# Kernel optimization log

Hardware: AMD Instinct MI355X
Metric: run time of the kernel (lower is better)

The kernel has to match this reference:

```python
import jax, jax.numpy as jnp
import numpy as np

N_NODES = 50000
N_EDGES = 1600000
IN_CH = 128
HID = 128
OUT_CH = 2
N_GRAPHS = 512
N_HID_LAYERS = 5  # first 5 SAGEConv+BN+ReLU blocks; 6th conv has no BN/act
EPS = 1e-5


def setup_inputs() -> dict:
    key = jax.random.key(0)
    ks = jax.random.split(key, 13)
    x = jax.random.normal(ks[0], (N_NODES, IN_CH), jnp.float32)
    edge_index = jax.random.randint(ks[1], (2, N_EDGES), 0, N_NODES)
    batch = jnp.sort(jax.random.randint(ks[2], (N_NODES,), 0, N_GRAPHS))
    s = 1.0 / np.sqrt(HID)
    # SAGEConv params for the 5 hidden layers (in==hid==128 so they stack)
    Wl = jax.random.normal(ks[3], (N_HID_LAYERS, HID, HID), jnp.float32) * s  # lin_l (neighbors)
    Wr = jax.random.normal(ks[4], (N_HID_LAYERS, HID, HID), jnp.float32) * s  # lin_r (root)
    b = jax.random.normal(ks[5], (N_HID_LAYERS, HID), jnp.float32) * s
    # BatchNorm (eval mode: running stats + affine)
    gamma = 1.0 + 0.1 * jax.random.normal(ks[6], (N_HID_LAYERS, HID), jnp.float32)
    beta = 0.1 * jax.random.normal(ks[7], (N_HID_LAYERS, HID), jnp.float32)
    rmean = 0.1 * jax.random.normal(ks[8], (N_HID_LAYERS, HID), jnp.float32)
    rvar = 0.5 + jax.random.uniform(ks[9], (N_HID_LAYERS, HID), dtype=jnp.float32)
    # final SAGEConv: hid -> out
    Wl_out = jax.random.normal(ks[10], (HID, OUT_CH), jnp.float32) * s
    Wr_out = jax.random.normal(ks[11], (HID, OUT_CH), jnp.float32) * s
    b_out = jax.random.normal(ks[12], (OUT_CH,), jnp.float32) * s
    return dict(x=x, Wl=Wl, Wr=Wr, b=b, gamma=gamma, beta=beta, rmean=rmean,
                rvar=rvar, Wl_out=Wl_out, Wr_out=Wr_out, b_out=b_out,
                edge_index=edge_index, batch=batch)


def reference(x, Wl, Wr, b, gamma, beta, rmean, rvar, Wl_out, Wr_out, b_out,
              edge_index, batch):
    src, dst = edge_index[0], edge_index[1]
    # in-degree for mean aggregation (shared across all layers)
    deg = jax.ops.segment_sum(jnp.ones((src.shape[0],), x.dtype), dst,
                              num_segments=N_NODES)
    inv_deg = (1.0 / jnp.maximum(deg, 1.0))[:, None]  # [N,1]

    def sage(h, Wl_, Wr_, b_):
        # PyG SAGEConv: lin_l(mean_{j in N(i)} x_j) + lin_r(x_i)
        agg = jax.ops.segment_sum(h[src], dst, num_segments=N_NODES) * inv_deg
        return agg @ Wl_ + h @ Wr_ + b_

    h = x
    for l in range(N_HID_LAYERS):
        h = sage(h, Wl[l], Wr[l], b[l])
        # BatchNorm1d in eval mode: affine with running stats
        h = (h - rmean[l]) * (gamma[l] * jax.lax.rsqrt(rvar[l] + EPS)) + beta[l]
        h = jax.nn.relu(h)
        # F.dropout(p=0.2, training=False) is identity in eval
    h = sage(h, Wl_out, Wr_out, b_out)  # [N, OUT_CH]
    # global_mean_pool over graphs
    gsum = jax.ops.segment_sum(h, batch, num_segments=N_GRAPHS)
    gcnt = jax.ops.segment_sum(jnp.ones((h.shape[0],), h.dtype), batch,
                               num_segments=N_GRAPHS)
    return gsum / jnp.maximum(gcnt, 1.0)[:, None]  # [N_GRAPHS, OUT_CH]
```

## Files before the change

### kernel.cpp

```cpp
#include <hip/hip_runtime.h>

#define HID 128
#define BN_EPS 1e-5f

typedef short bf16x8 __attribute__((ext_vector_type(8)));
typedef float f32x4 __attribute__((ext_vector_type(4)));

__device__ inline unsigned short f2b(float f) {
  unsigned int u = __float_as_uint(f);
  unsigned int r = (u + 0x7fffu + ((u >> 16) & 1u)) >> 16;
  return (unsigned short)r;
}
__device__ inline float bl(unsigned int v) { return __uint_as_float(v << 16); }
__device__ inline float bh(unsigned int v) { return __uint_as_float(v & 0xffff0000u); }


__global__ void k_bhist(const int* __restrict__ dst, int* __restrict__ bcnt, int e, int nb) {
  __shared__ int h[256];
  for (int i = threadIdx.x; i < 256; i += blockDim.x) h[i] = 0;
  __syncthreads();
  int stride = gridDim.x * blockDim.x;
  for (int i = blockIdx.x * blockDim.x + threadIdx.x; i < e; i += stride)
    atomicAdd(&h[dst[i] >> 8], 1);
  __syncthreads();
  for (int i = threadIdx.x; i < nb; i += blockDim.x)
    if (h[i]) atomicAdd(&bcnt[i], h[i]);
}

__global__ void k_bscan(const int* __restrict__ bcnt, int* __restrict__ base,
                        int* __restrict__ cur, int nb) {
  __shared__ int ws[4];
  int t = threadIdx.x;
  int v = (t < nb) ? bcnt[t] : 0;
  int lane = t & 63, wid = t >> 6;
  int x = v;
#pragma unroll
  for (int off = 1; off < 64; off <<= 1) {
    int y = __shfl_up(x, off, 64);
    if (lane >= off) x += y;
  }
  if (lane == 63) ws[wid] = x;
  __syncthreads();
  int add = 0;
  for (int w = 0; w < wid; ++w) add += ws[w];
  int incl = x + add;
  int excl = incl - v;
  if (t < nb) { base[t] = excl; cur[t] = excl; }
  if (t == nb - 1) base[nb] = incl;
}

__global__ void k_bscatter(const int* __restrict__ src, const int* __restrict__ dst,
                           int* __restrict__ cur, uint2* __restrict__ binned, int e) {
  __shared__ int bc[256];
  __shared__ int bo[256];
  int nchunk = (e + gridDim.x - 1) / gridDim.x;
  int c0 = blockIdx.x * nchunk;
  int c1 = min(c0 + nchunk, e);
  for (int i = threadIdx.x; i < 256; i += blockDim.x) bc[i] = 0;
  __syncthreads();
  for (int i = c0 + threadIdx.x; i < c1; i += blockDim.x)
    atomicAdd(&bc[dst[i] >> 8], 1);
  __syncthreads();
  for (int i = threadIdx.x; i < 256; i += blockDim.x) {
    int c = bc[i];
    bo[i] = c ? atomicAdd(&cur[i], c) : 0;
    bc[i] = 0;
  }
  __syncthreads();
  for (int i = c0 + threadIdx.x; i < c1; i += blockDim.x) {
    int d = dst[i];
    int b = d >> 8;
    int pos = bo[b] + atomicAdd(&bc[b], 1);
    binned[pos] = make_uint2((unsigned)src[i], (unsigned)d);
  }
}

__global__ __launch_bounds__(256) void k_bfill(
    const uint2* __restrict__ binned, const int* __restrict__ base,
    int* __restrict__ row_ptr, float* __restrict__ inv_deg,
    int* __restrict__ col, int n, int nb) {
  __shared__ int cnt[256];
  __shared__ int cur[256];
  __shared__ int ws[4];
  int b = blockIdx.x;
  int t = threadIdx.x;
  int n0 = b << 8;
  int e0 = base[b], e1 = base[b + 1];
  cnt[t] = 0;
  __syncthreads();
  for (int i = e0 + t; i < e1; i += 256)
    atomicAdd(&cnt[binned[i].y & 255], 1);
  __syncthreads();
  int v = cnt[t];
  int lane = t & 63, wid = t >> 6;
  int x = v;
#pragma unroll
  for (int off = 1; off < 64; off <<= 1) {
    int y = __shfl_up(x, off, 64);
    if (lane >= off) x += y;
  }
  if (lane == 63) ws[wid] = x;
  __syncthreads();
  int add = 0;
  for (int w = 0; w < wid; ++w) add += ws[w];
  int excl = x - v + add;
  int node = n0 + t;
  if (node < n) {
    row_ptr[node] = e0 + excl;
    inv_deg[node] = 1.0f / (float)max(v, 1);
  }
  cur[t] = e0 + excl;
  __syncthreads();
  for (int i = e0 + t; i < e1; i += 256) {
    uint2 pr = binned[i];
    int pos = atomicAdd(&cur[pr.y & 255], 1);
    col[pos] = (int)pr.x;
  }
  if (b == 0 && t == 0) row_ptr[n] = base[nb];
}


__global__ void k_prep(const float* __restrict__ x, unsigned short* __restrict__ xb,
                       const float* __restrict__ Wl, const float* __restrict__ Wr,
                       unsigned short* __restrict__ Wlt, unsigned short* __restrict__ Wrt,
                       const float* __restrict__ g, const float* __restrict__ be,
                       const float* __restrict__ rm, const float* __restrict__ rv,
                       float* __restrict__ sc, float* __restrict__ sh,
                       int n4, int wtot, int bn) {
  int i = blockIdx.x * blockDim.x + threadIdx.x;
  if (i < n4) {
    float4 v = ((const float4*)x)[i];
    unsigned int lo = (unsigned int)f2b(v.x) | ((unsigned int)f2b(v.y) << 16);
    unsigned int hi = (unsigned int)f2b(v.z) | ((unsigned int)f2b(v.w) << 16);
    ((uint2*)xb)[i] = make_uint2(lo, hi);
  } else if (i < n4 + wtot) {
    int j = i - n4;
    int mat = j >> 14, rem = j & 16383, nn = rem >> 7, kk = rem & 127;
    int sidx = (mat << 14) + (kk << 7) + nn;
    Wlt[j] = f2b(Wl[sidx]);
    Wrt[j] = f2b(Wr[sidx]);
  } else if (i < n4 + wtot + bn) {
    int j = i - n4 - wtot;
    float s = g[j] * rsqrtf(rv[j] + BN_EPS);
    sc[j] = s;
    sh[j] = be[j] - rm[j] * s;
  }
}


__global__ __launch_bounds__(256) void k_spmm_g(
    const unsigned short* __restrict__ hbsrc, const int* __restrict__ row_ptr,
    const int* __restrict__ col, const float* __restrict__ inv_deg,
    unsigned short* __restrict__ aggb, int n) {
  int node = blockIdx.x * 4 + (threadIdx.x >> 6);
  if (node >= n) return;
  int lane = threadIdx.x & 63;
  int slot = lane >> 4, c16 = lane & 15;
  int beg = row_ptr[node], end = row_ptr[node + 1];
  float a0 = 0, a1 = 0, a2 = 0, a3 = 0, a4 = 0, a5 = 0, a6 = 0, a7 = 0;
  const unsigned short* base = hbsrc + (c16 << 3);
  int e = beg;
  for (; e + 16 <= end; e += 16) {
    int s0 = col[e + slot];
    int s1 = col[e + 4 + slot];
    int s2 = col[e + 8 + slot];
    int s3 = col[e + 12 + slot];
    uint4 v0 = *(const uint4*)(base + ((size_t)s0 << 7));
    uint4 v1 = *(const uint4*)(base + ((size_t)s1 << 7));
    uint4 v2 = *(const uint4*)(base + ((size_t)s2 << 7));
    uint4 v3 = *(const uint4*)(base + ((size_t)s3 << 7));
    a0 += bl(v0.x); a1 += bh(v0.x); a2 += bl(v0.y); a3 += bh(v0.y);
    a4 += bl(v0.z); a5 += bh(v0.z); a6 += bl(v0.w); a7 += bh(v0.w);
    a0 += bl(v1.x); a1 += bh(v1.x); a2 += bl(v1.y); a3 += bh(v1.y);
    a4 += bl(v1.z); a5 += bh(v1.z); a6 += bl(v1.w); a7 += bh(v1.w);
    a0 += bl(v2.x); a1 += bh(v2.x); a2 += bl(v2.y); a3 += bh(v2.y);
    a4 += bl(v2.z); a5 += bh(v2.z); a6 += bl(v2.w); a7 += bh(v2.w);
    a0 += bl(v3.x); a1 += bh(v3.x); a2 += bl(v3.y); a3 += bh(v3.y);
    a4 += bl(v3.z); a5 += bh(v3.z); a6 += bl(v3.w); a7 += bh(v3.w);
  }
  for (; e < end; e += 4) {
    int idx = e + slot;
    if (idx < end) {
      int s = col[idx];
      uint4 v = *(const uint4*)(base + ((size_t)s << 7));
      a0 += bl(v.x); a1 += bh(v.x); a2 += bl(v.y); a3 += bh(v.y);
      a4 += bl(v.z); a5 += bh(v.z); a6 += bl(v.w); a7 += bh(v.w);
    }
  }
#pragma unroll
  for (int st = 16; st <= 32; st <<= 1) {
    a0 += __shfl_xor(a0, st); a1 += __shfl_xor(a1, st);
    a2 += __shfl_xor(a2, st); a3 += __shfl_xor(a3, st);
    a4 += __shfl_xor(a4, st); a5 += __shfl_xor(a5, st);
    a6 += __shfl_xor(a6, st); a7 += __shfl_xor(a7, st);
  }
  if (slot == 0) {
    float w = inv_deg[node];
    unsigned int p0 = (unsigned int)f2b(a0 * w) | ((unsigned int)f2b(a1 * w) << 16);
    unsigned int p1 = (unsigned int)f2b(a2 * w) | ((unsigned int)f2b(a3 * w) << 16);
    unsigned int p2 = (unsigned int)f2b(a4 * w) | ((unsigned int)f2b(a5 * w) << 16);
    unsigned int p3 = (unsigned int)f2b(a6 * w) | ((unsigned int)f2b(a7 * w) << 16);
    *(uint4*)(aggb + ((size_t)node << 7) + (c16 << 3)) = make_uint4(p0, p1, p2, p3);
  }
}


__global__ __launch_bounds__(256) void k_gemm3(
    const unsigned short* __restrict__ aggb,
    const unsigned short* __restrict__ hbsrc,
    const unsigned short* __restrict__ Wlt,
    const unsigned short* __restrict__ Wrt,
    const float* __restrict__ bias, const float* __restrict__ sc,
    const float* __restrict__ sh, unsigned short* __restrict__ hbo,
    int n, int ngroups) {
  int w = threadIdx.x >> 6;
  int lane = threadIdx.x & 63;
  int l15 = lane & 15, lhi = lane >> 4;

  bf16x8 aL[2][4], aR[2][4];
#pragma unroll
  for (int ms = 0; ms < 2; ++ms) {
    int row = (w << 5) + (ms << 4) + l15;
#pragma unroll
    for (int ks = 0; ks < 4; ++ks) {
      aL[ms][ks] = *(const bf16x8*)(Wlt + (row << 7) + (ks << 5) + (lhi << 3));
      aR[ms][ks] = *(const bf16x8*)(Wrt + (row << 7) + (ks << 5) + (lhi << 3));
    }
  }
  float4 bi[2], scv[2], shv[2];
#pragma unroll
  for (int ms = 0; ms < 2; ++ms) {
    int ch = (w << 5) + (ms << 4) + (lhi << 2);
    bi[ms] = *(const float4*)(bias + ch);
    scv[ms] = *(const float4*)(sc + ch);
    shv[ms] = *(const float4*)(sh + ch);
  }

  for (int g = blockIdx.x; g < ngroups; g += gridDim.x) {
    int node = (g << 4) + l15;
    bool ok = node < n;
    int nsafe = ok ? node : 0;
    const unsigned short* arow = aggb + ((size_t)nsafe << 7) + (lhi << 3);
    const unsigned short* hrow = hbsrc + ((size_t)nsafe << 7) + (lhi << 3);
    bf16x8 bA0 = *(const bf16x8*)(arow);
    bf16x8 bA1 = *(const bf16x8*)(arow + 32);
    bf16x8 bA2 = *(const bf16x8*)(arow + 64);
    bf16x8 bA3 = *(const bf16x8*)(arow + 96);
    bf16x8 bH0 = *(const bf16x8*)(hrow);
    bf16x8 bH1 = *(const bf16x8*)(hrow + 32);
    bf16x8 bH2 = *(const bf16x8*)(hrow + 64);
    bf16x8 bH3 = *(const bf16x8*)(hrow + 96);
    f32x4 acc[2];
#pragma unroll
    for (int ms = 0; ms < 2; ++ms) acc[ms] = (f32x4)(0.f);
#pragma unroll
    for (int ms = 0; ms < 2; ++ms) {
      acc[ms] = __builtin_amdgcn_mfma_f32_16x16x32_bf16(aL[ms][0], bA0, acc[ms], 0, 0, 0);
      acc[ms] = __builtin_amdgcn_mfma_f32_16x16x32_bf16(aL[ms][1], bA1, acc[ms], 0, 0, 0);
      acc[ms] = __builtin_amdgcn_mfma_f32_16x16x32_bf16(aL[ms][2], bA2, acc[ms], 0, 0, 0);
      acc[ms] = __builtin_amdgcn_mfma_f32_16x16x32_bf16(aL[ms][3], bA3, acc[ms], 0, 0, 0);
      acc[ms] = __builtin_amdgcn_mfma_f32_16x16x32_bf16(aR[ms][0], bH0, acc[ms], 0, 0, 0);
      acc[ms] = __builtin_amdgcn_mfma_f32_16x16x32_bf16(aR[ms][1], bH1, acc[ms], 0, 0, 0);
      acc[ms] = __builtin_amdgcn_mfma_f32_16x16x32_bf16(aR[ms][2], bH2, acc[ms], 0, 0, 0);
      acc[ms] = __builtin_amdgcn_mfma_f32_16x16x32_bf16(aR[ms][3], bH3, acc[ms], 0, 0, 0);
    }
    if (ok) {
#pragma unroll
      for (int ms = 0; ms < 2; ++ms) {
        int ch = (w << 5) + (ms << 4) + (lhi << 2);
        float o0 = fmaxf((acc[ms][0] + bi[ms].x) * scv[ms].x + shv[ms].x, 0.f);
        float o1 = fmaxf((acc[ms][1] + bi[ms].y) * scv[ms].y + shv[ms].y, 0.f);
        float o2 = fmaxf((acc[ms][2] + bi[ms].z) * scv[ms].z + shv[ms].z, 0.f);
        float o3 = fmaxf((acc[ms][3] + bi[ms].w) * scv[ms].w + shv[ms].w, 0.f);
        unsigned int lo = (unsigned int)f2b(o0) | ((unsigned int)f2b(o1) << 16);
        unsigned int hi = (unsigned int)f2b(o2) | ((unsigned int)f2b(o3) << 16);
        *(uint2*)(hbo + ((size_t)node << 7) + ch) = make_uint2(lo, hi);
      }
    }
  }
}


__global__ void k_pq(const unsigned short* __restrict__ hb, const float* __restrict__ Wl_out,
                     const float* __restrict__ Wr_out, float* __restrict__ p,
                     float* __restrict__ q, int n) {
  int node = blockIdx.x * 4 + (threadIdx.x >> 6);
  if (node >= n) return;
  int lane = threadIdx.x & 63;
  unsigned int hv = *(const unsigned int*)(hb + ((size_t)node << 7) + (lane << 1));
  float hx = bl(hv), hy = bh(hv);
  float4 wl = *(const float4*)(Wl_out + (lane << 2));
  float4 wr = *(const float4*)(Wr_out + (lane << 2));
  float p0 = hx * wl.x + hy * wl.z;
  float p1 = hx * wl.y + hy * wl.w;
  float q0 = hx * wr.x + hy * wr.z;
  float q1 = hx * wr.y + hy * wr.w;
#pragma unroll
  for (int off = 32; off > 0; off >>= 1) {
    p0 += __shfl_xor(p0, off, 64);
    p1 += __shfl_xor(p1, off, 64);
    q0 += __shfl_xor(q0, off, 64);
    q1 += __shfl_xor(q1, off, 64);
  }
  if (lane == 0) {
    *(float2*)(p + (size_t)node * 2) = make_float2(p0, p1);
    *(float2*)(q + (size_t)node * 2) = make_float2(q0, q1);
  }
}

__global__ void k_spmm2p(const float* __restrict__ p, const float* __restrict__ q,
                         const int* __restrict__ row_ptr, const int* __restrict__ col,
                         const float* __restrict__ inv_deg, const float* __restrict__ b_out,
                         const int* __restrict__ batch, float* __restrict__ out,
                         float* __restrict__ gcnt, int n) {
  int i = blockIdx.x * blockDim.x + threadIdx.x;
  int lane = threadIdx.x & 63;
  bool valid = i < n;
  float o0 = 0.f, o1 = 0.f;
  int g = -1;
  if (valid) {
    int beg = row_ptr[i], end = row_ptr[i + 1];
    float a0 = 0.f, a1 = 0.f, b0 = 0.f, b1 = 0.f;
    int e = beg;
    for (; e + 2 <= end; e += 2) {
      float2 v0 = *(const float2*)(p + (size_t)col[e] * 2);
      float2 v1 = *(const float2*)(p + (size_t)col[e + 1] * 2);
      a0 += v0.x; a1 += v0.y; b0 += v1.x; b1 += v1.y;
    }
    if (e < end) {
      float2 v = *(const float2*)(p + (size_t)col[e] * 2);
      a0 += v.x; a1 += v.y;
    }
    float w = inv_deg[i];
    float2 qv = *(const float2*)(q + (size_t)i * 2);
    o0 = (a0 + b0) * w + qv.x + b_out[0];
    o1 = (a1 + b1) * w + qv.y + b_out[1];
    g = batch[i];
  }
  float s0 = o0, s1 = o1;
#pragma unroll
  for (int off = 1; off < 64; off <<= 1) {
    float y0 = __shfl_up(s0, off, 64);
    float y1 = __shfl_up(s1, off, 64);
    if (lane >= off) { s0 += y0; s1 += y1; }
  }
  int gprev = __shfl_up(g, 1, 64);
  int gnext = __shfl_down(g, 1, 64);
  bool is_start = (lane == 0) || (g != gprev);
  bool is_end = valid && ((lane == 63) || (g != gnext));
  int startl = is_start ? lane : 0;
#pragma unroll
  for (int off = 1; off < 64; off <<= 1) {
    int y = __shfl_up(startl, off, 64);
    if (lane >= off) startl = max(startl, y);
  }
  int prevl = startl > 0 ? startl - 1 : 0;
  float t0 = __shfl(s0, prevl, 64);
  float t1 = __shfl(s1, prevl, 64);
  if (is_end) {
    float p0 = startl > 0 ? t0 : 0.f;
    float p1 = startl > 0 ? t1 : 0.f;
    atomicAdd(&out[g * 2], s0 - p0);
    atomicAdd(&out[g * 2 + 1], s1 - p1);
    atomicAdd(&gcnt[g], (float)(lane - startl + 1));
  }
}

__global__ void k_div(float* __restrict__ out, const float* __restrict__ gcnt, int ng) {
  int i = blockIdx.x * blockDim.x + threadIdx.x;
  if (i < ng * 2) out[i] /= fmaxf(gcnt[i >> 1], 1.0f);
}


extern "C" void kernel_launch(void* const* d_in, const int* in_sizes, int n_in,
                              void* d_out, int out_size, void* d_ws, size_t ws_size,
                              hipStream_t stream) {
  const float* x = (const float*)d_in[0];
  const float* Wl = (const float*)d_in[1];
  const float* Wr = (const float*)d_in[2];
  const float* b = (const float*)d_in[3];
  const float* gamma = (const float*)d_in[4];
  const float* beta = (const float*)d_in[5];
  const float* rmean = (const float*)d_in[6];
  const float* rvar = (const float*)d_in[7];
  const float* Wl_out = (const float*)d_in[8];
  const float* Wr_out = (const float*)d_in[9];
  const float* b_out = (const float*)d_in[10];
  const int* eidx = (const int*)d_in[11];
  const int* batch = (const int*)d_in[12];

  const int N = in_sizes[0] / HID;
  const int E = in_sizes[11] / 2;
  const int L = in_sizes[1] / (HID * HID);
  const int NG = out_size / 2;
  const int NB = (N + 255) >> 8;
  const int NGRP = (N + 15) >> 4;
  const int* src = eidx;
  const int* dst = eidx + E;

  char* ws = (char*)d_ws;
  size_t off = 0;
  auto alloc = [&](size_t bytes) {
    void* ptr = ws + off;
    off += (bytes + 255) & ~(size_t)255;
    return ptr;
  };
  int* row_ptr = (int*)alloc((size_t)(N + 1) * 4);
  int* bcnt = (int*)alloc((size_t)NB * 4);
  int* bbase = (int*)alloc((size_t)(NB + 1) * 4);
  int* bcur = (int*)alloc((size_t)NB * 4);
  int* col = (int*)alloc((size_t)E * 4);
  float* inv_deg = (float*)alloc((size_t)N * 4);
  unsigned short* xb = (unsigned short*)alloc((size_t)N * HID * 2);
  unsigned short* hb0 = (unsigned short*)alloc((size_t)N * HID * 2);
  unsigned short* hb1 = (unsigned short*)alloc((size_t)N * HID * 2);
  unsigned short* aggb = (unsigned short*)alloc((size_t)N * HID * 2);
  unsigned short* Wlt = (unsigned short*)alloc((size_t)L * HID * HID * 2);
  unsigned short* Wrt = (unsigned short*)alloc((size_t)L * HID * HID * 2);
  float* sc = (float*)alloc((size_t)L * HID * 4);
  float* sh = (float*)alloc((size_t)L * HID * 4);
  float* p = (float*)alloc((size_t)N * 2 * 4);
  float* q = (float*)alloc((size_t)N * 2 * 4);
  float* gcnt = (float*)alloc((size_t)NG * 4);
  uint2* binned = (uint2*)alloc((size_t)E * 8);

  hipMemsetAsync(bcnt, 0, (size_t)NB * 4, stream);
  k_bhist<<<256, 256, 0, stream>>>(dst, bcnt, E, NB);
  k_bscan<<<1, 256, 0, stream>>>(bcnt, bbase, bcur, NB);
  k_bscatter<<<256, 256, 0, stream>>>(src, dst, bcur, binned, E);
  k_bfill<<<NB, 256, 0, stream>>>(binned, bbase, row_ptr, inv_deg, col, N, NB);

  const int n4 = N * HID / 4;
  const int wtot = L * HID * HID;
  const int bn = L * HID;
  k_prep<<<(n4 + wtot + bn + 255) / 256, 256, 0, stream>>>(
      x, xb, Wl, Wr, Wlt, Wrt, gamma, beta, rmean, rvar, sc, sh, n4, wtot, bn);

  const unsigned short* hin = xb;
  for (int l = 0; l < L; ++l) {
    unsigned short* hnext = (l & 1) ? hb1 : hb0;
    k_spmm_g<<<(N + 3) / 4, 256, 0, stream>>>(hin, row_ptr, col, inv_deg, aggb, N);
    k_gemm3<<<512, 256, 0, stream>>>(
        aggb, hin, Wlt + (size_t)l * HID * HID, Wrt + (size_t)l * HID * HID,
        b + (size_t)l * HID, sc + (size_t)l * HID, sh + (size_t)l * HID,
        hnext, N, NGRP);
    hin = hnext;
  }
  k_pq<<<(N + 3) / 4, 256, 0, stream>>>(hin, Wl_out, Wr_out, p, q, N);
  hipMemsetAsync(d_out, 0, (size_t)out_size * 4, stream);
  hipMemsetAsync(gcnt, 0, (size_t)NG * 4, stream);
  k_spmm2p<<<(N + 255) / 256, 256, 0, stream>>>(
      p, q, row_ptr, col, inv_deg, b_out, batch, (float*)d_out, gcnt, N);
  k_div<<<(NG * 2 + 255) / 256, 256, 0, stream>>>((float*)d_out, gcnt, NG);
}
```

Measured before the change: 446.2 us.

## Pack binned edges to 32 bits, halve SpMM blocks, dual-group GEMM loop

The CSR binning buffer now stores each edge as one 32-bit word: the source index in the low 16 bits and the destination's offset within its bin in the high bits. This halves traffic in the scatter and fill kernels but assumes node indices fit in 16 bits. The SpMM gather kernel uses 128-thread blocks (two nodes each) instead of 256. The fused GEMM kernel processes two 16-node groups per iteration, issuing both groups' loads and interleaved MFMA chains together for more memory- and instruction-level parallelism, at the cost of more registers.

```diff
diff --git a/kernel.cpp b/kernel.cpp
--- a/kernel.cpp
+++ b/kernel.cpp
@@ -50,7 +50,7 @@
 }
 
 __global__ void k_bscatter(const int* __restrict__ src, const int* __restrict__ dst,
-                           int* __restrict__ cur, uint2* __restrict__ binned, int e) {
+                           int* __restrict__ cur, unsigned int* __restrict__ binned, int e) {
   __shared__ int bc[256];
   __shared__ int bo[256];
   int nchunk = (e + gridDim.x - 1) / gridDim.x;
@@ -71,12 +71,12 @@
     int d = dst[i];
     int b = d >> 8;
     int pos = bo[b] + atomicAdd(&bc[b], 1);
-    binned[pos] = make_uint2((unsigned)src[i], (unsigned)d);
+    binned[pos] = (unsigned)src[i] | ((unsigned)(d & 255) << 16);
   }
 }
 
 __global__ __launch_bounds__(256) void k_bfill(
-    const uint2* __restrict__ binned, const int* __restrict__ base,
+    const unsigned int* __restrict__ binned, const int* __restrict__ base,
     int* __restrict__ row_ptr, float* __restrict__ inv_deg,
     int* __restrict__ col, int n, int nb) {
   __shared__ int cnt[256];
@@ -89,7 +89,7 @@
   cnt[t] = 0;
   __syncthreads();
   for (int i = e0 + t; i < e1; i += 256)
-    atomicAdd(&cnt[binned[i].y & 255], 1);
+    atomicAdd(&cnt[binned[i] >> 16], 1);
   __syncthreads();
   int v = cnt[t];
   int lane = t & 63, wid = t >> 6;
@@ -112,9 +112,9 @@
   cur[t] = e0 + excl;
   __syncthreads();
   for (int i = e0 + t; i < e1; i += 256) {
-    uint2 pr = binned[i];
-    int pos = atomicAdd(&cur[pr.y & 255], 1);
-    col[pos] = (int)pr.x;
+    unsigned int pr = binned[i];
+    int pos = atomicAdd(&cur[pr >> 16], 1);
+    col[pos] = (int)(pr & 0xffffu);
   }
   if (b == 0 && t == 0) row_ptr[n] = base[nb];
 }
@@ -148,11 +148,11 @@
 }
 
 
-__global__ __launch_bounds__(256) void k_spmm_g(
+__global__ __launch_bounds__(128) void k_spmm_g(
     const unsigned short* __restrict__ hbsrc, const int* __restrict__ row_ptr,
     const int* __restrict__ col, const float* __restrict__ inv_deg,
     unsigned short* __restrict__ aggb, int n) {
-  int node = blockIdx.x * 4 + (threadIdx.x >> 6);
+  int node = blockIdx.x * 2 + (threadIdx.x >> 6);
   if (node >= n) return;
   int lane = threadIdx.x & 63;
   int slot = lane >> 4, c16 = lane & 15;
@@ -236,45 +236,63 @@
     shv[ms] = *(const float4*)(sh + ch);
   }
 
-  for (int g = blockIdx.x; g < ngroups; g += gridDim.x) {
-    int node = (g << 4) + l15;
-    bool ok = node < n;
-    int nsafe = ok ? node : 0;
-    const unsigned short* arow = aggb + ((size_t)nsafe << 7) + (lhi << 3);
-    const unsigned short* hrow = hbsrc + ((size_t)nsafe << 7) + (lhi << 3);
-    bf16x8 bA0 = *(const bf16x8*)(arow);
-    bf16x8 bA1 = *(const bf16x8*)(arow + 32);
-    bf16x8 bA2 = *(const bf16x8*)(arow + 64);
-    bf16x8 bA3 = *(const bf16x8*)(arow + 96);
-    bf16x8 bH0 = *(const bf16x8*)(hrow);
-    bf16x8 bH1 = *(const bf16x8*)(hrow + 32);
-    bf16x8 bH2 = *(const bf16x8*)(hrow + 64);
-    bf16x8 bH3 = *(const bf16x8*)(hrow + 96);
-    f32x4 acc[2];
-#pragma unroll
-    for (int ms = 0; ms < 2; ++ms) acc[ms] = (f32x4)(0.f);
+  for (int g0 = blockIdx.x * 2; g0 < ngroups; g0 += gridDim.x * 2) {
+    int g1 = g0 + 1;
+    int nodeA = (g0 << 4) + l15;
+    bool okA = nodeA < n;
+    bool okB = (g1 < ngroups);
+    int nodeB = okB ? (g1 << 4) + l15 : nodeA;
+    okB = okB && nodeB < n;
+    int nsA = okA ? nodeA : 0;
+    int nsB = okB ? nodeB : 0;
+    const unsigned short* arowA = aggb + ((size_t)nsA << 7) + (lhi << 3);
+    const unsigned short* hrowA = hbsrc + ((size_t)nsA << 7) + (lhi << 3);
+    const unsigned short* arowB = aggb + ((size_t)nsB << 7) + (lhi << 3);
+    const unsigned short* hrowB = hbsrc + ((size_t)nsB << 7) + (lhi << 3);
+    bf16x8 bA[4], bH[4], cA[4], cH[4];
+#pragma unroll
+    for (int ks = 0; ks < 4; ++ks) {
+      bA[ks] = *(const bf16x8*)(arowA + (ks << 5));
+      bH[ks] = *(const bf16x8*)(hrowA + (ks << 5));
+      cA[ks] = *(const bf16x8*)(arowB + (ks << 5));
+      cH[ks] = *(const bf16x8*)(hrowB + (ks << 5));
+    }
+    f32x4 acc0[2], acc1[2];
+#pragma unroll
+    for (int ms = 0; ms < 2; ++ms) { acc0[ms] = (f32x4)(0.f); acc1[ms] = (f32x4)(0.f); }
 #pragma unroll
     for (int ms = 0; ms < 2; ++ms) {
-      acc[ms] = __builtin_amdgcn_mfma_f32_16x16x32_bf16(aL[ms][0], bA0, acc[ms], 0, 0, 0);
-      acc[ms] = __builtin_amdgcn_mfma_f32_16x16x32_bf16(aL[ms][1], bA1, acc[ms], 0, 0, 0);
-      acc[ms] = __builtin_amdgcn_mfma_f32_16x16x32_bf16(aL[ms][2], bA2, acc[ms], 0, 0, 0);
-      acc[ms] = __builtin_amdgcn_mfma_f32_16x16x32_bf16(aL[ms][3], bA3, acc[ms], 0, 0, 0);
-      acc[ms] = __builtin_amdgcn_mfma_f32_16x16x32_bf16(aR[ms][0], bH0, acc[ms], 0, 0, 0);
-      acc[ms] = __builtin_amdgcn_mfma_f32_16x16x32_bf16(aR[ms][1], bH1, acc[ms], 0, 0, 0);
-      acc[ms] = __builtin_amdgcn_mfma_f32_16x16x32_bf16(aR[ms][2], bH2, acc[ms], 0, 0, 0);
-      acc[ms] = __builtin_amdgcn_mfma_f32_16x16x32_bf16(aR[ms][3], bH3, acc[ms], 0, 0, 0);
-    }
-    if (ok) {
-#pragma unroll
-      for (int ms = 0; ms < 2; ++ms) {
-        int ch = (w << 5) + (ms << 4) + (lhi << 2);
-        float o0 = fmaxf((acc[ms][0] + bi[ms].x) * scv[ms].x + shv[ms].x, 0.f);
-        float o1 = fmaxf((acc[ms][1] + bi[ms].y) * scv[ms].y + shv[ms].y, 0.f);
-        float o2 = fmaxf((acc[ms][2] + bi[ms].z) * scv[ms].z + shv[ms].z, 0.f);
-        float o3 = fmaxf((acc[ms][3] + bi[ms].w) * scv[ms].w + shv[ms].w, 0.f);
+#pragma unroll
+      for (int ks = 0; ks < 4; ++ks) {
+        acc0[ms] = __builtin_amdgcn_mfma_f32_16x16x32_bf16(aL[ms][ks], bA[ks], acc0[ms], 0, 0, 0);
+        acc1[ms] = __builtin_amdgcn_mfma_f32_16x16x32_bf16(aL[ms][ks], cA[ks], acc1[ms], 0, 0, 0);
+      }
+#pragma unroll
+      for (int ks = 0; ks < 4; ++ks) {
+        acc0[ms] = __builtin_amdgcn_mfma_f32_16x16x32_bf16(aR[ms][ks], bH[ks], acc0[ms], 0, 0, 0);
+        acc1[ms] = __builtin_amdgcn_mfma_f32_16x16x32_bf16(aR[ms][ks], cH[ks], acc1[ms], 0, 0, 0);
+      }
+    }
+#pragma unroll
+    for (int ms = 0; ms < 2; ++ms) {
+      int ch = (w << 5) + (ms << 4) + (lhi << 2);
+      if (okA) {
+        float o0 = fmaxf((acc0[ms][0] + bi[ms].x) * scv[ms].x + shv[ms].x, 0.f);
+        float o1 = fmaxf((acc0[ms][1] + bi[ms].y) * scv[ms].y + shv[ms].y, 0.f);
+        float o2 = fmaxf((acc0[ms][2] + bi[ms].z) * scv[ms].z + shv[ms].z, 0.f);
+        float o3 = fmaxf((acc0[ms][3] + bi[ms].w) * scv[ms].w + shv[ms].w, 0.f);
         unsigned int lo = (unsigned int)f2b(o0) | ((unsigned int)f2b(o1) << 16);
         unsigned int hi = (unsigned int)f2b(o2) | ((unsigned int)f2b(o3) << 16);
-        *(uint2*)(hbo + ((size_t)node << 7) + ch) = make_uint2(lo, hi);
+        *(uint2*)(hbo + ((size_t)nodeA << 7) + ch) = make_uint2(lo, hi);
+      }
+      if (okB) {
+        float o0 = fmaxf((acc1[ms][0] + bi[ms].x) * scv[ms].x + shv[ms].x, 0.f);
+        float o1 = fmaxf((acc1[ms][1] + bi[ms].y) * scv[ms].y + shv[ms].y, 0.f);
+        float o2 = fmaxf((acc1[ms][2] + bi[ms].z) * scv[ms].z + shv[ms].z, 0.f);
+        float o3 = fmaxf((acc1[ms][3] + bi[ms].w) * scv[ms].w + shv[ms].w, 0.f);
+        unsigned int lo = (unsigned int)f2b(o0) | ((unsigned int)f2b(o1) << 16);
+        unsigned int hi = (unsigned int)f2b(o2) | ((unsigned int)f2b(o3) << 16);
+        *(uint2*)(hbo + ((size_t)nodeB << 7) + ch) = make_uint2(lo, hi);
       }
     }
   }
@@ -422,7 +440,7 @@
   float* p = (float*)alloc((size_t)N * 2 * 4);
   float* q = (float*)alloc((size_t)N * 2 * 4);
   float* gcnt = (float*)alloc((size_t)NG * 4);
-  uint2* binned = (uint2*)alloc((size_t)E * 8);
+  unsigned int* binned = (unsigned int*)alloc((size_t)E * 4);
 
   hipMemsetAsync(bcnt, 0, (size_t)NB * 4, stream);
   k_bhist<<<256, 256, 0, stream>>>(dst, bcnt, E, NB);
@@ -439,7 +457,7 @@
   const unsigned short* hin = xb;
   for (int l = 0; l < L; ++l) {
     unsigned short* hnext = (l & 1) ? hb1 : hb0;
-    k_spmm_g<<<(N + 3) / 4, 256, 0, stream>>>(hin, row_ptr, col, inv_deg, aggb, N);
+    k_spmm_g<<<(N + 1) / 2, 128, 0, stream>>>(hin, row_ptr, col, inv_deg, aggb, N);
     k_gemm3<<<512, 256, 0, stream>>>(
         aggb, hin, Wlt + (size_t)l * HID * HID, Wrt + (size_t)l * HID * HID,
         b + (size_t)l * HID, sc + (size_t)l * HID, sh + (size_t)l * HID,
```

Measured after the change: 453.1 us. No clear change (+1.5%).
